# Optimization experiments

Measured on AMD Instinct MI355X. Metric: run time of the kernel, lower is better.

The kernel has to match this reference:

```python
import jax, jax.numpy as jnp
import numpy as np

N_NODES = 50000
NODE_DIM = 256
HIDDEN = 512
N_EDGES = 500000


def setup_inputs() -> dict:
    key = jax.random.key(0)
    k1, k2, k3, k4 = jax.random.split(key, 4)
    x = jax.random.normal(k1, (N_NODES, NODE_DIM), dtype=jnp.float32)
    edge_index = jax.random.randint(k2, (2, N_EDGES), 0, N_NODES, dtype=jnp.int64)
    in_dim = 2 * NODE_DIM  # concat mode
    W1 = jax.random.normal(k3, (in_dim, HIDDEN), dtype=jnp.float32) / np.sqrt(in_dim)
    b1 = jnp.zeros((HIDDEN,), dtype=jnp.float32)
    W2 = jax.random.normal(k4, (HIDDEN, 1), dtype=jnp.float32) / np.sqrt(HIDDEN)
    b2 = jnp.zeros((1,), dtype=jnp.float32)
    return {"x": x, "edge_index": edge_index, "W1": W1, "b1": b1, "W2": W2, "b2": b2}


def reference(x, edge_index, W1, b1, W2, b2):
    row, col = edge_index[0], edge_index[1]
    # concat mode: edge_feat [E, 2*node_dim]
    edge_feat = jnp.concatenate([x[row], x[col]], axis=1)
    h = jax.nn.relu(edge_feat @ W1 + b1)  # [E, hidden]
    score = (h @ W2 + b2).squeeze(-1)     # [E]
    return score
```

## Files before the change

kernel.cpp:

```cpp
#include <hip/hip_runtime.h>
#include <hip/hip_bf16.h>

#define N_NODES  50000
#define NODE_DIM 256
#define HIDDEN   512
#define N_EDGES  500000
#define M_PAD    50048
#define NCAT     1024
#define KDIM     256
#define NB       391
#define CAP      1536
#define NSLOTS   (NB * CAP)
#define QSCALE   30.238095f
#define DSCALE   0.033070866f
#define DUMMY    0xFFFFFFFF00000000ULL

typedef __attribute__((ext_vector_type(4))) unsigned short ushort4v;
typedef __attribute__((ext_vector_type(8))) __bf16 bf16x8;
typedef __attribute__((ext_vector_type(4))) float f32x4;
typedef __attribute__((ext_vector_type(4))) unsigned int uint4v;
typedef __attribute__((ext_vector_type(2))) unsigned int uint2v;
typedef __attribute__((ext_vector_type(2))) unsigned long long ull2;
typedef __attribute__((ext_vector_type(2))) float float2v;

__device__ __forceinline__ unsigned short f2bf(float f) {
  unsigned int u = __builtin_bit_cast(unsigned int, f);
  u += 0x7fffu + ((u >> 16) & 1u);
  return (unsigned short)(u >> 16);
}

__device__ __forceinline__ void gload16(const void* g, void* l) {
  __builtin_amdgcn_global_load_lds(
      (__attribute__((address_space(1))) void*)(g),
      (__attribute__((address_space(3))) void*)(l),
      16, 0, 0);
}

__global__ void prep_kernel(const float* __restrict__ x, unsigned short* __restrict__ xb,
                            const float* __restrict__ W1, unsigned short* __restrict__ wt,
                            int* __restrict__ counts, unsigned long long* __restrict__ slots) {
  const int b = blockIdx.x;
  if (b < 2048) {
    const int total4 = M_PAD * NODE_DIM / 4;
    const int valid4 = N_NODES * NODE_DIM / 4;
    for (int i = b * 256 + threadIdx.x; i < total4; i += 2048 * 256) {
      ushort4v o;
      if (i < valid4) {
        float4 v = ((const float4*)x)[i];
        o[0] = f2bf(v.x); o[1] = f2bf(v.y); o[2] = f2bf(v.z); o[3] = f2bf(v.w);
      } else {
        o[0] = 0; o[1] = 0; o[2] = 0; o[3] = 0;
      }
      ((ushort4v*)xb)[i] = o;
    }
  } else if (b < 3072) {
    int i = (b - 2048) * 256 + threadIdx.x;
    int n = i >> 8;
    int k = i & 255;
    int srow = (n >= HIDDEN) ? (NODE_DIM + k) : k;
    int scol = n & (HIDDEN - 1);
    wt[i] = f2bf(W1[srow * HIDDEN + scol]);
  } else if (b == 3072) {
    for (int i = threadIdx.x; i < NB; i += 256) counts[i] = 0;
  } else {
    int bb = b - 3073;
    for (int i = bb * 256 + threadIdx.x; i < NSLOTS; i += 512 * 256)
      slots[i] = DUMMY;
  }
}

__global__ __launch_bounds__(256, 2) void gemm_kernel(
    const unsigned short* __restrict__ Xb,
    const unsigned short* __restrict__ Wt,
    const float* __restrict__ b1,
    unsigned short* __restrict__ CbA,
    signed char* __restrict__ CbB) {
  __shared__ unsigned short As[128 * 32];
  __shared__ unsigned short Bs[128 * 32];
  const int t = threadIdx.x;
  const int w = t >> 6;
  const int lane = t & 63;
  const int bid = blockIdx.x;
  const int xcd = bid & 7;
  const int loc = bid >> 3;
  const int tileN = loc / 49;
  const int tileM = xcd * 49 + (loc - tileN * 49);
  if (tileM >= 391) return;
  const int wm = w >> 1, wn = w & 1;

  f32x4 acc[4][4] = {};

  const int rowA0 = tileM * 128;
  const int rowB0 = tileN * 128;
  const int rstage = t >> 2;
  const int cstage = (t & 3) * 8;

  for (int kk = 0; kk < KDIM; kk += 32) {
#pragma unroll
    for (int i = 0; i < 2; ++i) {
      const unsigned short* srcA = Xb + (size_t)(rowA0 + i * 64 + rstage) * KDIM + kk + cstage;
      gload16(srcA, (char*)As + i * 4096 + w * 1024);
      const unsigned short* srcB = Wt + (size_t)(rowB0 + i * 64 + rstage) * KDIM + kk + cstage;
      gload16(srcB, (char*)Bs + i * 4096 + w * 1024);
    }
    __syncthreads();

    bf16x8 a[4], bfr[4];
#pragma unroll
    for (int fm = 0; fm < 4; ++fm)
      a[fm] = *(const bf16x8*)&As[(wm * 64 + fm * 16 + (lane & 15)) * 32 + (lane >> 4) * 8];
#pragma unroll
    for (int fn = 0; fn < 4; ++fn)
      bfr[fn] = *(const bf16x8*)&Bs[(wn * 64 + fn * 16 + (lane & 15)) * 32 + (lane >> 4) * 8];
#pragma unroll
    for (int fm = 0; fm < 4; ++fm)
#pragma unroll
      for (int fn = 0; fn < 4; ++fn)
        acc[fm][fn] = __builtin_amdgcn_mfma_f32_16x16x32_bf16(a[fm], bfr[fn], acc[fm][fn], 0, 0, 0);
    __syncthreads();
  }

  const int row0 = tileM * 128 + wm * 64;
  if (tileN < 4) {
    const int col0 = tileN * 128 + wn * 64;
    float b1v[4];
#pragma unroll
    for (int fn = 0; fn < 4; ++fn) b1v[fn] = b1[col0 + fn * 16 + (lane & 15)];
#pragma unroll
    for (int fm = 0; fm < 4; ++fm)
#pragma unroll
      for (int fn = 0; fn < 4; ++fn)
#pragma unroll
        for (int r = 0; r < 4; ++r) {
          int row = row0 + fm * 16 + (lane >> 4) * 4 + r;
          int col = col0 + fn * 16 + (lane & 15);
          CbA[(size_t)row * HIDDEN + col] = f2bf(acc[fm][fn][r] + b1v[fn]);
        }
  } else {
    const int col0 = (tileN - 4) * 128 + wn * 64;
#pragma unroll
    for (int fm = 0; fm < 4; ++fm)
#pragma unroll
      for (int fn = 0; fn < 4; ++fn)
#pragma unroll
        for (int r = 0; r < 4; ++r) {
          int row = row0 + fm * 16 + (lane >> 4) * 4 + r;
          int col = col0 + fn * 16 + (lane & 15);
          float v = fminf(fmaxf(acc[fm][fn][r], -4.2f), 4.2f);
          CbB[(size_t)row * HIDDEN + col] = (signed char)__float2int_rn(v * QSCALE);
        }
  }
}

__global__ void scatter_kernel(const int* __restrict__ ei, int* __restrict__ counts,
                               unsigned long long* __restrict__ slots) {
  __shared__ int h[NB];
  __shared__ int bbase[NB];
  const int chunk = (N_EDGES + gridDim.x - 1) / gridDim.x;
  const int e0 = blockIdx.x * chunk;
  const int e1 = min(e0 + chunk, N_EDGES);
  for (int i = threadIdx.x; i < NB; i += blockDim.x) h[i] = 0;
  __syncthreads();
  for (int e = e0 + threadIdx.x; e < e1; e += blockDim.x)
    atomicAdd(&h[ei[e] >> 7], 1);
  __syncthreads();
  for (int i = threadIdx.x; i < NB; i += blockDim.x) {
    int c = h[i];
    bbase[i] = c ? atomicAdd(&counts[i], c) : 0;
    h[i] = 0;
  }
  __syncthreads();
  for (int e = e0 + threadIdx.x; e < e1; e += blockDim.x) {
    int r = ei[e];
    int c = ei[N_EDGES + e];
    int b = r >> 7;
    int idx = bbase[b] + atomicAdd(&h[b], 1);
    slots[(size_t)b * CAP + idx] =
        (unsigned long long)r | ((unsigned long long)c << 16) | ((unsigned long long)e << 32);
  }
}

__device__ __forceinline__ float2v edge_mlp_pk(uint4v ua, uint2v ub,
                                               const float2v* w2p) {
  const float2v dscale2 = {DSCALE, DSCALE};
  const float2v zero2 = {0.f, 0.f};
  float2v acc = zero2;
#pragma unroll
  for (int j = 0; j < 4; ++j) {
    unsigned int au = ua[j];
    float2v a;
    a[0] = __builtin_bit_cast(float, au << 16);
    a[1] = __builtin_bit_cast(float, au & 0xffff0000u);
    unsigned int ubw = ub[j >> 1];
    int sh = (j & 1) * 16;
    float2v q;
    q[0] = (float)(int)(signed char)(ubw >> sh);
    q[1] = (float)(int)(signed char)(ubw >> (sh + 8));
    float2v h = __builtin_elementwise_fma(q, dscale2, a);
    h = __builtin_elementwise_max(h, zero2);
    acc = __builtin_elementwise_fma(h, w2p[j], acc);
  }
  return acc;
}

__global__ __launch_bounds__(256) void edge_kernel(
    const unsigned short* __restrict__ CbA,
    const signed char* __restrict__ CbB,
    const unsigned long long* __restrict__ slots,
    const float* __restrict__ W2,
    const float* __restrict__ b2,
    float* __restrict__ out) {
  const int lane = threadIdx.x & 63;
  const int xcd = blockIdx.x & 7;
  const int lwid = (blockIdx.x >> 3) * 4 + (threadIdx.x >> 6);
  const int nlw = (gridDim.x >> 3) * 4;
  const int per_xcd = NSLOTS / 8;
  const int pbase = xcd * per_xcd;
  const int base = lane * 8;

  float2v w2p[4];
  {
    float4 u0 = *(const float4*)&W2[base];
    float4 u1 = *(const float4*)&W2[base + 4];
    w2p[0] = (float2v){u0.x, u0.y};
    w2p[1] = (float2v){u0.z, u0.w};
    w2p[2] = (float2v){u1.x, u1.y};
    w2p[3] = (float2v){u1.z, u1.w};
  }
  const float bias2 = b2[0];

  const int pend = pbase + per_xcd;
  for (int p = pbase + lwid * 4; p < pend; p += nlw * 4) {
    ull2 rrA = *(const ull2*)(slots + p);
    ull2 rrB = *(const ull2*)(slots + p + 2);
    const int id0 = (int)(rrA[0] >> 32);
    const int id1 = (int)(rrA[1] >> 32);
    const int id2 = (int)(rrB[0] >> 32);
    const int id3 = (int)(rrB[1] >> 32);
    if ((id0 & id1 & id2 & id3) < 0) continue;
    const int r0 = (int)(rrA[0] & 0xFFFF), c0 = (int)((rrA[0] >> 16) & 0xFFFF);
    const int r1 = (int)(rrA[1] & 0xFFFF), c1 = (int)((rrA[1] >> 16) & 0xFFFF);
    const int r2 = (int)(rrB[0] & 0xFFFF), c2 = (int)((rrB[0] >> 16) & 0xFFFF);
    const int r3 = (int)(rrB[1] & 0xFFFF), c3 = (int)((rrB[1] >> 16) & 0xFFFF);
    uint4v ua0 = *(const uint4v*)(CbA + (size_t)r0 * HIDDEN + base);
    uint2v ub0 = *(const uint2v*)(CbB + (size_t)c0 * HIDDEN + base);
    uint4v ua1 = *(const uint4v*)(CbA + (size_t)r1 * HIDDEN + base);
    uint2v ub1 = *(const uint2v*)(CbB + (size_t)c1 * HIDDEN + base);
    uint4v ua2 = *(const uint4v*)(CbA + (size_t)r2 * HIDDEN + base);
    uint2v ub2 = *(const uint2v*)(CbB + (size_t)c2 * HIDDEN + base);
    uint4v ua3 = *(const uint4v*)(CbA + (size_t)r3 * HIDDEN + base);
    uint2v ub3 = *(const uint2v*)(CbB + (size_t)c3 * HIDDEN + base);

    float2v a0 = edge_mlp_pk(ua0, ub0, w2p);
    float2v a1 = edge_mlp_pk(ua1, ub1, w2p);
    float2v a2 = edge_mlp_pk(ua2, ub2, w2p);
    float2v a3 = edge_mlp_pk(ua3, ub3, w2p);
    float acc0 = a0[0] + a0[1];
    float acc1 = a1[0] + a1[1];
    float acc2 = a2[0] + a2[1];
    float acc3 = a3[0] + a3[1];

#pragma unroll
    for (int off = 32; off >= 16; off >>= 1) {
      acc0 += __shfl_xor(acc0, off, 64);
      acc1 += __shfl_xor(acc1, off, 64);
      acc2 += __shfl_xor(acc2, off, 64);
      acc3 += __shfl_xor(acc3, off, 64);
    }
    const int q = lane >> 4;
    float v = (q == 0) ? acc0 : (q == 1) ? acc1 : (q == 2) ? acc2 : acc3;
#pragma unroll
    for (int off = 8; off; off >>= 1)
      v += __shfl_xor(v, off, 64);
    if ((lane & 15) == 0) {
      const int idq = (q == 0) ? id0 : (q == 1) ? id1 : (q == 2) ? id2 : id3;
      if (idq >= 0) out[idq] = v + bias2;
    }
  }
}

extern "C" void kernel_launch(void* const* d_in, const int* in_sizes, int n_in,
                              void* d_out, int out_size, void* d_ws, size_t ws_size,
                              hipStream_t stream) {
  const float* x  = (const float*)d_in[0];
  const int*   ei = (const int*)d_in[1];
  const float* W1 = (const float*)d_in[2];
  const float* b1 = (const float*)d_in[3];
  const float* W2 = (const float*)d_in[4];
  const float* b2 = (const float*)d_in[5];
  float* out = (float*)d_out;

  char* ws = (char*)d_ws;
  const size_t xb_bytes  = (size_t)M_PAD * KDIM * 2;
  const size_t wt_bytes  = (size_t)NCAT * KDIM * 2;
  const size_t cbA_bytes = (size_t)M_PAD * HIDDEN * 2;
  const size_t cbB_bytes = (size_t)M_PAD * HIDDEN;
  unsigned short* xb  = (unsigned short*)ws;
  unsigned short* wt  = (unsigned short*)(ws + xb_bytes);
  unsigned short* cbA = (unsigned short*)(ws + xb_bytes + wt_bytes);
  signed char*    cbB = (signed char*)(ws + xb_bytes + wt_bytes + cbA_bytes);
  char* tail = ws + xb_bytes + wt_bytes + cbA_bytes + cbB_bytes;
  int* counts = (int*)tail;
  unsigned long long* slots = (unsigned long long*)(tail + 4096);

  hipLaunchKernelGGL(prep_kernel, dim3(3585), dim3(256), 0, stream, x, xb, W1, wt, counts, slots);
  hipLaunchKernelGGL(gemm_kernel, dim3(392 * 8), dim3(256), 0, stream,
                     xb, wt, b1, cbA, cbB);
  hipLaunchKernelGGL(scatter_kernel, dim3(512), dim3(256), 0, stream, ei, counts, slots);
  hipLaunchKernelGGL(edge_kernel, dim3(2048), dim3(256), 0, stream, cbA, cbB, slots, W2, b2, out);
}
```

Measured before the change: 149.2 us.

## Merge scatter into GEMM launch and double K-step per LDS stage

Folds the edge scatter/bucketing kernel into the GEMM launch as extra trailing blocks. This removes one kernel launch and lets the scatter work overlap with the GEMM tail. The GEMM K tile also grows from 32 to 64, which halves the number of barrier-separated load stages. In exchange, shared memory per block rises to about 35KB, which could limit occupancy.

```diff
diff --git a/kernel.cpp b/kernel.cpp
--- a/kernel.cpp
+++ b/kernel.cpp
@@ -14,6 +14,8 @@
 #define QSCALE   30.238095f
 #define DSCALE   0.033070866f
 #define DUMMY    0xFFFFFFFF00000000ULL
+#define GEMM_BLKS (392 * 8)
+#define SCAT_BLKS 512
 
 typedef __attribute__((ext_vector_type(4))) unsigned short ushort4v;
 typedef __attribute__((ext_vector_type(8))) __bf16 bf16x8;
@@ -74,13 +76,46 @@
     const unsigned short* __restrict__ Wt,
     const float* __restrict__ b1,
     unsigned short* __restrict__ CbA,
-    signed char* __restrict__ CbB) {
-  __shared__ unsigned short As[128 * 32];
-  __shared__ unsigned short Bs[128 * 32];
+    signed char* __restrict__ CbB,
+    const int* __restrict__ ei,
+    int* __restrict__ counts,
+    unsigned long long* __restrict__ slots) {
+  __shared__ unsigned short As[128 * 64];
+  __shared__ unsigned short Bs[128 * 64];
+  __shared__ int h[NB];
+  __shared__ int bbase[NB];
   const int t = threadIdx.x;
+  const int bid = blockIdx.x;
+
+  if (bid >= GEMM_BLKS) {
+    const int sb = bid - GEMM_BLKS;
+    const int chunk = (N_EDGES + SCAT_BLKS - 1) / SCAT_BLKS;
+    const int e0 = sb * chunk;
+    const int e1 = min(e0 + chunk, N_EDGES);
+    for (int i = t; i < NB; i += 256) h[i] = 0;
+    __syncthreads();
+    for (int e = e0 + t; e < e1; e += 256)
+      atomicAdd(&h[ei[e] >> 7], 1);
+    __syncthreads();
+    for (int i = t; i < NB; i += 256) {
+      int c = h[i];
+      bbase[i] = c ? atomicAdd(&counts[i], c) : 0;
+      h[i] = 0;
+    }
+    __syncthreads();
+    for (int e = e0 + t; e < e1; e += 256) {
+      int r = ei[e];
+      int c = ei[N_EDGES + e];
+      int b = r >> 7;
+      int idx = bbase[b] + atomicAdd(&h[b], 1);
+      slots[(size_t)b * CAP + idx] =
+          (unsigned long long)r | ((unsigned long long)c << 16) | ((unsigned long long)e << 32);
+    }
+    return;
+  }
+
   const int w = t >> 6;
   const int lane = t & 63;
-  const int bid = blockIdx.x;
   const int xcd = bid & 7;
   const int loc = bid >> 3;
   const int tileN = loc / 49;
@@ -92,31 +127,34 @@
 
   const int rowA0 = tileM * 128;
   const int rowB0 = tileN * 128;
-  const int rstage = t >> 2;
-  const int cstage = (t & 3) * 8;
-
-  for (int kk = 0; kk < KDIM; kk += 32) {
-#pragma unroll
-    for (int i = 0; i < 2; ++i) {
-      const unsigned short* srcA = Xb + (size_t)(rowA0 + i * 64 + rstage) * KDIM + kk + cstage;
+  const int rstage = t >> 3;
+  const int cstage = (t & 7) * 8;
+
+  for (int kk = 0; kk < KDIM; kk += 64) {
+#pragma unroll
+    for (int i = 0; i < 4; ++i) {
+      const unsigned short* srcA = Xb + (size_t)(rowA0 + i * 32 + rstage) * KDIM + kk + cstage;
       gload16(srcA, (char*)As + i * 4096 + w * 1024);
-      const unsigned short* srcB = Wt + (size_t)(rowB0 + i * 64 + rstage) * KDIM + kk + cstage;
+      const unsigned short* srcB = Wt + (size_t)(rowB0 + i * 32 + rstage) * KDIM + kk + cstage;
       gload16(srcB, (char*)Bs + i * 4096 + w * 1024);
     }
     __syncthreads();
 
-    bf16x8 a[4], bfr[4];
-#pragma unroll
-    for (int fm = 0; fm < 4; ++fm)
-      a[fm] = *(const bf16x8*)&As[(wm * 64 + fm * 16 + (lane & 15)) * 32 + (lane >> 4) * 8];
-#pragma unroll
-    for (int fn = 0; fn < 4; ++fn)
-      bfr[fn] = *(const bf16x8*)&Bs[(wn * 64 + fn * 16 + (lane & 15)) * 32 + (lane >> 4) * 8];
-#pragma unroll
-    for (int fm = 0; fm < 4; ++fm)
+#pragma unroll
+    for (int kk2 = 0; kk2 < 64; kk2 += 32) {
+      bf16x8 a[4], bfr[4];
+#pragma unroll
+      for (int fm = 0; fm < 4; ++fm)
+        a[fm] = *(const bf16x8*)&As[(wm * 64 + fm * 16 + (lane & 15)) * 64 + kk2 + (lane >> 4) * 8];
 #pragma unroll
       for (int fn = 0; fn < 4; ++fn)
-        acc[fm][fn] = __builtin_amdgcn_mfma_f32_16x16x32_bf16(a[fm], bfr[fn], acc[fm][fn], 0, 0, 0);
+        bfr[fn] = *(const bf16x8*)&Bs[(wn * 64 + fn * 16 + (lane & 15)) * 64 + kk2 + (lane >> 4) * 8];
+#pragma unroll
+      for (int fm = 0; fm < 4; ++fm)
+#pragma unroll
+        for (int fn = 0; fn < 4; ++fn)
+          acc[fm][fn] = __builtin_amdgcn_mfma_f32_16x16x32_bf16(a[fm], bfr[fn], acc[fm][fn], 0, 0, 0);
+    }
     __syncthreads();
   }
 
@@ -149,34 +187,6 @@
           float v = fminf(fmaxf(acc[fm][fn][r], -4.2f), 4.2f);
           CbB[(size_t)row * HIDDEN + col] = (signed char)__float2int_rn(v * QSCALE);
         }
-  }
-}
-
-__global__ void scatter_kernel(const int* __restrict__ ei, int* __restrict__ counts,
-                               unsigned long long* __restrict__ slots) {
-  __shared__ int h[NB];
-  __shared__ int bbase[NB];
-  const int chunk = (N_EDGES + gridDim.x - 1) / gridDim.x;
-  const int e0 = blockIdx.x * chunk;
-  const int e1 = min(e0 + chunk, N_EDGES);
-  for (int i = threadIdx.x; i < NB; i += blockDim.x) h[i] = 0;
-  __syncthreads();
-  for (int e = e0 + threadIdx.x; e < e1; e += blockDim.x)
-    atomicAdd(&h[ei[e] >> 7], 1);
-  __syncthreads();
-  for (int i = threadIdx.x; i < NB; i += blockDim.x) {
-    int c = h[i];
-    bbase[i] = c ? atomicAdd(&counts[i], c) : 0;
-    h[i] = 0;
-  }
-  __syncthreads();
-  for (int e = e0 + threadIdx.x; e < e1; e += blockDim.x) {
-    int r = ei[e];
-    int c = ei[N_EDGES + e];
-    int b = r >> 7;
-    int idx = bbase[b] + atomicAdd(&h[b], 1);
-    slots[(size_t)b * CAP + idx] =
-        (unsigned long long)r | ((unsigned long long)c << 16) | ((unsigned long long)e << 32);
   }
 }
 
@@ -304,8 +314,7 @@
   unsigned long long* slots = (unsigned long long*)(tail + 4096);
 
   hipLaunchKernelGGL(prep_kernel, dim3(3585), dim3(256), 0, stream, x, xb, W1, wt, counts, slots);
-  hipLaunchKernelGGL(gemm_kernel, dim3(392 * 8), dim3(256), 0, stream,
-                     xb, wt, b1, cbA, cbB);
-  hipLaunchKernelGGL(scatter_kernel, dim3(512), dim3(256), 0, stream, ei, counts, slots);
+  hipLaunchKernelGGL(gemm_kernel, dim3(GEMM_BLKS + SCAT_BLKS), dim3(256), 0, stream,
+                     xb, wt, b1, cbA, cbB, ei, counts, slots);
   hipLaunchKernelGGL(edge_kernel, dim3(2048), dim3(256), 0, stream, cbA, cbB, slots, W2, b2, out);
 }
```

Result: faster. 137.9 us (-7.6%).
